# Kernel optimization log

Hardware: AMD Instinct MI355X
Metric: run time of the kernel (lower is better)

## Reference

```python
import jax, jax.numpy as jnp
import numpy as np

D = 256       # video_dim == gcn_dims == interaction_dim
FD = 512      # forward_dim = 2 * interaction_dim
UPDATE_RATE = 0.5


def setup_inputs() -> dict:
    key = jax.random.key(0)
    ks = jax.random.split(key, 20)
    T, N = 768, 384
    s = lambda *sh: 1.0 / np.sqrt(sh[-1])
    return {
        "video_features": jax.random.normal(ks[0], (T, D), jnp.float32),
        "text_features": jax.random.normal(ks[1], (N, D), jnp.float32),
        "video_position_embedding": jax.random.normal(ks[2], (T, D), jnp.float32),
        "text_position_embedding": jax.random.normal(ks[3], (N, D), jnp.float32),
        # VideoEncoder conv1d (out=D, in=D, k=3)
        "conv_w": jax.random.normal(ks[4], (D, D, 3), jnp.float32) * (1.0 / np.sqrt(D * 3)),
        "conv_b": jax.random.normal(ks[5], (D,), jnp.float32) * 0.01,
        # TextGnnEncoder
        "bil_w": jax.random.normal(ks[6], (D, D), jnp.float32) * s(D, D),
        "lin_w": jax.random.normal(ks[7], (D, D), jnp.float32) * s(D, D),
        "lin_b": jax.random.normal(ks[8], (D,), jnp.float32) * 0.01,
        # PairInteraction
        "W1": jax.random.normal(ks[9], (FD, D), jnp.float32) * s(FD, D),
        "b1": jax.random.normal(ks[10], (FD,), jnp.float32) * 0.01,
        "W2": jax.random.normal(ks[11], (FD, D), jnp.float32) * s(FD, D),
        "Wi": jax.random.normal(ks[12], (D, FD), jnp.float32) * s(D, FD),
        "bi": jax.random.normal(ks[13], (D,), jnp.float32) * 0.01,
        # amplifier generators (Linear(interaction_dim, 1))
        "wt": jax.random.normal(ks[14], (D,), jnp.float32) * s(D,),
        "bt": jax.random.normal(ks[15], (1,), jnp.float32) * 0.01,
        "wv": jax.random.normal(ks[16], (D,), jnp.float32) * s(D,),
        "bv": jax.random.normal(ks[17], (1,), jnp.float32) * 0.01,
    }


def _forward(video_features, text_features, video_position_embedding, text_position_embedding,
             conv_w, conv_b, bil_w, lin_w, lin_b, W1, b1, W2, Wi, bi, wt, bt, wv, bv):
    T, N = video_features.shape[0], text_features.shape[0]
    input_video, input_text = video_features, text_features

    v = video_features + video_position_embedding          # (T, D)
    t = text_features + text_position_embedding            # (N, D)

    # VideoEncoder: Conv1d(k=3, pad=1) over time, then ReLU (dropout=0 in eval)
    x = v.T[None]                                           # (1, D, T)
    x = jax.lax.conv_general_dilated(x, conv_w, (1,), [(1, 1)],
                                     dimension_numbers=("NCH", "OIH", "NCH"))
    v = jax.nn.relu(x[0] + conv_b[:, None]).T               # (T, D)

    # TextGnnEncoder
    tn = t / jnp.maximum(jnp.linalg.norm(t, axis=1, keepdims=True), 1e-12)  # L2 normalize rows
    edges = (tn @ bil_w.T) @ tn.T                            # (N, N)
    weights = jax.nn.sigmoid(jnp.mean(edges, axis=1, keepdims=True))        # (N, 1)
    t = weights * (tn @ lin_w.T + lin_b)                     # (N, D)

    # PairInteraction: broadcast add + ReLU + Linear
    f1 = v @ W1.T + b1                                       # (T, FD)
    f2 = t @ W2.T                                            # (N, FD)
    h = jax.nn.relu(f1[:, None, :] + f2[None, :, :])         # (T, N, FD)
    imap = jnp.einsum("tnf,of->tno", h, Wi) + bi             # (T, N, D)

    # dual softmax attention pooling
    text_att = jax.nn.softmax(imap @ wt + bt, axis=1)        # (T, N), softmax over N
    text_context = jnp.einsum("tn,nd->td", text_att, t)      # (T, D)
    video_att = jax.nn.softmax(imap @ wv + bv, axis=0)       # (T, N), softmax over T
    video_context = jnp.einsum("tn,td->nd", video_att, v)    # (N, D)

    ur = UPDATE_RATE
    t_out = video_context * ur + t * (1.0 - ur) + input_text
    v_out = text_context * ur + v * (1.0 - ur) + input_video
    return v_out, t_out


def reference(video_features, text_features, video_position_embedding, text_position_embedding,
              conv_w, conv_b, bil_w, lin_w, lin_b, W1, b1, W2, Wi, bi, wt, bt, wv, bv):
    return _forward(video_features, text_features, video_position_embedding, text_position_embedding,
                    conv_w, conv_b, bil_w, lin_w, lin_b, W1, b1, W2, Wi, bi, wt, bt, wv, bv)
```

## Files before the change

kernel.cpp:

```cpp
#include <hip/hip_runtime.h>
#include <math.h>

#define D  256
#define T  768
#define N  384
#define FD 512

#define DOT4(A,B) ((A).x*(B).x + (A).y*(B).y + (A).z*(B).z + (A).w*(B).w)

__global__ __launch_bounds__(256) void k_front(
    const float* __restrict__ vf, const float* __restrict__ vpos,
    const float* __restrict__ cw, const float* __restrict__ cb,
    const float* __restrict__ tf, const float* __restrict__ tpos,
    const float* __restrict__ Wi, const float* __restrict__ wt,
    const float* __restrict__ wv,
    float* __restrict__ ve, float* __restrict__ tn,
    float* __restrict__ ut, float* __restrict__ uv)
{
    __shared__ float As[34][68];
    __shared__ float Bs[3][32][68];
    const int b = blockIdx.x, tid = threadIdx.x;

    if (b < 192) {
        const int t0 = (b >> 3) * 32;
        const int o0 = (b & 7) * 32;
        const int p  = tid >> 4;
        const int oA = tid & 15;
        float acc00 = 0.f, acc01 = 0.f, acc10 = 0.f, acc11 = 0.f;

        for (int c = 0; c < 4; ++c) {
            const int i0 = c << 6;
            __syncthreads();
#pragma unroll
            for (int s = 0; s < 3; ++s) {
                int u = tid + (s << 8);
                if (u < 544) {
                    int r = u >> 4, uq = u & 15;
                    int gr = t0 - 1 + r;
                    float4 v = make_float4(0.f, 0.f, 0.f, 0.f);
                    if (gr >= 0 && gr < T) {
                        float4 a = *(const float4*)&vf[gr*D + i0 + uq*4];
                        float4 pz = *(const float4*)&vpos[gr*D + i0 + uq*4];
                        v = make_float4(a.x+pz.x, a.y+pz.y, a.z+pz.z, a.w+pz.w);
                    }
                    *(float4*)&As[r][uq*4] = v;
                }
            }
#pragma unroll
            for (int s = 0; s < 6; ++s) {
                int u = tid + (s << 8);
                int oc = u / 48, uq = u - oc * 48;
                float4 v = *(const float4*)&cw[(o0 + oc)*768 + i0*3 + uq*4];
                int j0 = uq * 4;
                Bs[(j0    ) % 3][oc][(j0    ) / 3] = v.x;
                Bs[(j0 + 1) % 3][oc][(j0 + 1) / 3] = v.y;
                Bs[(j0 + 2) % 3][oc][(j0 + 2) / 3] = v.z;
                Bs[(j0 + 3) % 3][oc][(j0 + 3) / 3] = v.w;
            }
            __syncthreads();
#pragma unroll 4
            for (int i4 = 0; i4 < 16; ++i4) {
                float4 ar0 = *(const float4*)&As[2*p    ][i4*4];
                float4 ar1 = *(const float4*)&As[2*p + 1][i4*4];
                float4 ar2 = *(const float4*)&As[2*p + 2][i4*4];
                float4 ar3 = *(const float4*)&As[2*p + 3][i4*4];
                float4 b00 = *(const float4*)&Bs[0][oA   ][i4*4];
                float4 b01 = *(const float4*)&Bs[0][oA+16][i4*4];
                float4 b10 = *(const float4*)&Bs[1][oA   ][i4*4];
                float4 b11 = *(const float4*)&Bs[1][oA+16][i4*4];
                float4 b20 = *(const float4*)&Bs[2][oA   ][i4*4];
                float4 b21 = *(const float4*)&Bs[2][oA+16][i4*4];
                acc00 += DOT4(ar0,b00) + DOT4(ar1,b10) + DOT4(ar2,b20);
                acc01 += DOT4(ar0,b01) + DOT4(ar1,b11) + DOT4(ar2,b21);
                acc10 += DOT4(ar1,b00) + DOT4(ar2,b10) + DOT4(ar3,b20);
                acc11 += DOT4(ar1,b01) + DOT4(ar2,b11) + DOT4(ar3,b21);
            }
        }
        const float bia = cb[o0 + oA], bib = cb[o0 + oA + 16];
        const int t = t0 + 2*p;
        ve[t*D + o0 + oA]          = fmaxf(acc00 + bia, 0.f);
        ve[t*D + o0 + oA + 16]     = fmaxf(acc01 + bib, 0.f);
        ve[(t+1)*D + o0 + oA]      = fmaxf(acc10 + bia, 0.f);
        ve[(t+1)*D + o0 + oA + 16] = fmaxf(acc11 + bib, 0.f);
    } else if (b < 288) {
        const int wid = tid >> 6, lane = tid & 63;
        const int r = (b - 192)*4 + wid;
        float v[4]; float ss = 0.f;
#pragma unroll
        for (int kk = 0; kk < 4; ++kk) {
            v[kk] = tf[r*D + lane + 64*kk] + tpos[r*D + lane + 64*kk];
            ss += v[kk]*v[kk];
        }
#pragma unroll
        for (int off = 1; off < 64; off <<= 1) ss += __shfl_xor(ss, off);
        float inv = 1.0f / fmaxf(sqrtf(ss), 1e-12f);
#pragma unroll
        for (int kk = 0; kk < 4; ++kk) tn[r*D + lane + 64*kk] = v[kk] * inv;
    } else {
        float* wsm = &As[0][0];
        const int which = b - 288;
        const float* w = (which < 2) ? wt : wv;
        float* u = (which < 2) ? ut : uv;
        const int f = ((which & 1) << 8) + tid;
        wsm[tid] = w[tid];
        __syncthreads();
        float s = 0.f;
#pragma unroll 4
        for (int d = 0; d < D; ++d) s += wsm[d] * Wi[d*FD + f];
        u[f] = s;
    }
}

__global__ __launch_bounds__(256) void k_mid(
    const float* __restrict__ ve, const float* __restrict__ W1,
    const float* __restrict__ b1, const float* __restrict__ tn,
    const float* __restrict__ bil, const float* __restrict__ lin_w,
    const float* __restrict__ lin_b,
    float* __restrict__ f1, float* __restrict__ q, float* __restrict__ tl)
{
    __shared__ float As[32][68];
    __shared__ float Bs[32][68];
    const int b = blockIdx.x, tid = threadIdx.x;

    if (b < 384) {
        const int t0 = (b >> 4) * 32;
        const int f0 = (b & 15) * 32;
        const int tA = tid >> 4, fA = tid & 15;
        float acc00 = 0.f, acc01 = 0.f, acc10 = 0.f, acc11 = 0.f;
        for (int c = 0; c < 4; ++c) {
            const int d0 = c << 6;
            __syncthreads();
            const int kc = tid & 63, g = tid >> 6;
#pragma unroll
            for (int it = 0; it < 8; ++it) {
                int tt = g + it*4;
                As[tt][kc] = ve[(t0 + tt)*D + d0 + kc];
                Bs[tt][kc] = W1[(f0 + tt)*D + d0 + kc];
            }
            __syncthreads();
#pragma unroll
            for (int kc4 = 0; kc4 < 16; ++kc4) {
                float4 a0 = *(const float4*)&As[tA][kc4*4];
                float4 a1 = *(const float4*)&As[tA+16][kc4*4];
                float4 b0 = *(const float4*)&Bs[fA][kc4*4];
                float4 b1 = *(const float4*)&Bs[fA+16][kc4*4];
                acc00 += DOT4(a0, b0); acc01 += DOT4(a0, b1);
                acc10 += DOT4(a1, b0); acc11 += DOT4(a1, b1);
            }
        }
        const float bia = b1[f0 + fA], bib = b1[f0 + fA + 16];
        f1[(t0 + tA)*FD + f0 + fA]           = acc00 + bia;
        f1[(t0 + tA)*FD + f0 + fA + 16]      = acc01 + bib;
        f1[(t0 + tA + 16)*FD + f0 + fA]      = acc10 + bia;
        f1[(t0 + tA + 16)*FD + f0 + fA + 16] = acc11 + bib;
    } else if (b < 392) {
        float* tb = &As[0][0];
        float (*qp)[32] = (float(*)[32])&Bs[0][0];
        const int bq = b - 384;
        float s = 0.f;
#pragma unroll 8
        for (int n = 0; n < N; ++n) s += tn[n*D + tid];
        tb[tid] = s * (1.0f / (float)N);
        __syncthreads();
        const int o = tid & 31, dg = tid >> 5;
        float p = 0.f;
#pragma unroll 8
        for (int d = dg*32; d < dg*32 + 32; ++d) p += tb[d] * bil[d*D + bq*32 + o];
        qp[dg][o] = p;
        __syncthreads();
        if (tid < 32) {
            float acc = 0.f;
#pragma unroll
            for (int kk = 0; kk < 8; ++kk) acc += qp[kk][tid];
            q[bq*32 + tid] = acc;
        }
    } else {
        const int bb = b - 392;
        const int n0 = (bb >> 3) * 32;
        const int o0 = (bb & 7) * 32;
        const int tA = tid >> 4, oA = tid & 15;
        float acc00 = 0.f, acc01 = 0.f, acc10 = 0.f, acc11 = 0.f;
        for (int c = 0; c < 4; ++c) {
            const int d0 = c << 6;
            __syncthreads();
            const int kc = tid & 63, g = tid >> 6;
#pragma unroll
            for (int it = 0; it < 8; ++it) {
                int tt = g + it*4;
                As[tt][kc] = tn[(n0 + tt)*D + d0 + kc];
                Bs[tt][kc] = lin_w[(o0 + tt)*D + d0 + kc];
            }
            __syncthreads();
#pragma unroll
            for (int kc4 = 0; kc4 < 16; ++kc4) {
                float4 a0 = *(const float4*)&As[tA][kc4*4];
                float4 a1 = *(const float4*)&As[tA+16][kc4*4];
                float4 b0 = *(const float4*)&Bs[oA][kc4*4];
                float4 b1 = *(const float4*)&Bs[oA+16][kc4*4];
                acc00 += DOT4(a0, b0); acc01 += DOT4(a0, b1);
                acc10 += DOT4(a1, b0); acc11 += DOT4(a1, b1);
            }
        }
        const float bia = lin_b[o0 + oA], bib = lin_b[o0 + oA + 16];
        tl[(n0 + tA)*D + o0 + oA]           = acc00 + bia;
        tl[(n0 + tA)*D + o0 + oA + 16]      = acc01 + bib;
        tl[(n0 + tA + 16)*D + o0 + oA]      = acc10 + bia;
        tl[(n0 + tA + 16)*D + o0 + oA + 16] = acc11 + bib;
    }
}

__global__ __launch_bounds__(256) void k_f2(
    const float* __restrict__ tn, const float* __restrict__ q,
    const float* __restrict__ tl, const float* __restrict__ W2,
    float* __restrict__ tg, float* __restrict__ f2)
{
    __shared__ float As[32][68];
    __shared__ float Bs[32][68];
    __shared__ float wsm[32];
    __shared__ float qs[D];
    const int tid = threadIdx.x;
    const int n0 = (blockIdx.x >> 4) * 32;
    const int f0 = (blockIdx.x & 15) * 32;

    qs[tid] = q[tid];
    __syncthreads();
    {
        const int r = tid >> 3, j = tid & 7;
        const float* row = tn + (n0 + r)*D + j*32;
        float p = 0.f;
#pragma unroll
        for (int m4 = 0; m4 < 8; ++m4) {
            float4 a = *(const float4*)&row[m4*4];
            float4 qq = *(const float4*)&qs[j*32 + m4*4];
            p += DOT4(a, qq);
        }
        p += __shfl_xor(p, 1); p += __shfl_xor(p, 2); p += __shfl_xor(p, 4);
        if (j == 0) wsm[r] = 1.0f / (1.0f + expf(-p));
    }
    __syncthreads();

    const int tA = tid >> 4, fA = tid & 15;
    float acc00 = 0.f, acc01 = 0.f, acc10 = 0.f, acc11 = 0.f;
    for (int c = 0; c < 4; ++c) {
        const int d0 = c << 6;
        __syncthreads();
        const int kc = tid & 63, g = tid >> 6;
#pragma unroll
        for (int it = 0; it < 8; ++it) {
            int tt = g + it*4;
            float av = wsm[tt] * tl[(n0 + tt)*D + d0 + kc];
            As[tt][kc] = av;
            if (f0 == 0) tg[(n0 + tt)*D + d0 + kc] = av;
            Bs[tt][kc] = W2[(f0 + tt)*D + d0 + kc];
        }
        __syncthreads();
#pragma unroll
        for (int kc4 = 0; kc4 < 16; ++kc4) {
            float4 a0 = *(const float4*)&As[tA][kc4*4];
            float4 a1 = *(const float4*)&As[tA+16][kc4*4];
            float4 b0 = *(const float4*)&Bs[fA][kc4*4];
            float4 b1 = *(const float4*)&Bs[fA+16][kc4*4];
            acc00 += DOT4(a0, b0); acc01 += DOT4(a0, b1);
            acc10 += DOT4(a1, b0); acc11 += DOT4(a1, b1);
        }
    }
    f2[(n0 + tA)*FD + f0 + fA]           = acc00;
    f2[(n0 + tA)*FD + f0 + fA + 16]      = acc01;
    f2[(n0 + tA + 16)*FD + f0 + fA]      = acc10;
    f2[(n0 + tA + 16)*FD + f0 + fA + 16] = acc11;
}

__global__ __launch_bounds__(256) void k_score(
    const float* __restrict__ f1, const float* __restrict__ f2,
    const float* __restrict__ ut, const float* __restrict__ uv,
    float* __restrict__ stp, float* __restrict__ svp)
{
    __shared__ float f1s[64][132];
    __shared__ float f2s[32][132];
    __shared__ float us_t[128];
    __shared__ float us_v[128];
    const int tid = threadIdx.x;
    const int t0 = blockIdx.x * 64, n0 = blockIdx.y * 32, c = blockIdx.z;

    if (tid < 128) { us_t[tid] = ut[c*128 + tid]; us_v[tid] = uv[c*128 + tid]; }
#pragma unroll
    for (int s = 0; s < 8; ++s) {
        int j = tid + (s << 8);
        int r = j >> 5, c4 = (j & 31) * 4;
        *(float4*)&f1s[r][c4] = *(const float4*)&f1[(t0 + r)*FD + c*128 + c4];
    }
#pragma unroll
    for (int s = 0; s < 4; ++s) {
        int j = tid + (s << 8);
        int r = j >> 5, c4 = (j & 31) * 4;
        *(float4*)&f2s[r][c4] = *(const float4*)&f2[(n0 + r)*FD + c*128 + c4];
    }
    __syncthreads();

    const int ti = tid >> 4, ni = tid & 15;
    float at[4][2] = {{0.f,0.f},{0.f,0.f},{0.f,0.f},{0.f,0.f}};
    float av[4][2] = {{0.f,0.f},{0.f,0.f},{0.f,0.f},{0.f,0.f}};

#pragma unroll 4
    for (int fq = 0; fq < 32; ++fq) {
        float utv[4], uvv[4], a[4][4], bb[2][4];
        *(float4*)utv   = *(const float4*)&us_t[fq*4];
        *(float4*)uvv   = *(const float4*)&us_v[fq*4];
        *(float4*)a[0]  = *(const float4*)&f1s[ti     ][fq*4];
        *(float4*)a[1]  = *(const float4*)&f1s[ti + 16][fq*4];
        *(float4*)a[2]  = *(const float4*)&f1s[ti + 32][fq*4];
        *(float4*)a[3]  = *(const float4*)&f1s[ti + 48][fq*4];
        *(float4*)bb[0] = *(const float4*)&f2s[ni     ][fq*4];
        *(float4*)bb[1] = *(const float4*)&f2s[ni + 16][fq*4];
#pragma unroll
        for (int e = 0; e < 4; ++e) {
#pragma unroll
            for (int m = 0; m < 4; ++m) {
#pragma unroll
                for (int mn = 0; mn < 2; ++mn) {
                    float h = fmaxf(a[m][e] + bb[mn][e], 0.f);
                    at[m][mn] += h * utv[e];
                    av[m][mn] += h * uvv[e];
                }
            }
        }
    }
    float* stz = stp + c * (T*N);
    float* svz = svp + c * (N*T);
#pragma unroll
    for (int m = 0; m < 4; ++m) {
        const int t = t0 + ti + 16*m;
#pragma unroll
        for (int mn = 0; mn < 2; ++mn) {
            const int n = n0 + ni + 16*mn;
            stz[t*N + n] = at[m][mn];
            svz[n*T + t] = av[m][mn];
        }
    }
}

__global__ __launch_bounds__(256) void k_att(
    const float* __restrict__ stp, const float* __restrict__ svp,
    const float* __restrict__ tg, const float* __restrict__ ve,
    const float* __restrict__ vf, const float* __restrict__ tf,
    float* __restrict__ out_v, float* __restrict__ out_t)
{
    __shared__ float attb[768][4];
    __shared__ float red[4][4];
    __shared__ float ptA[4][4][64];
    __shared__ float ptB[4][4][64];
    const int tid = threadIdx.x;
    const int oo = tid & 63, g = tid >> 6;

    if (blockIdx.x < 384) {
        const int bx = blockIdx.x >> 1, h = blockIdx.x & 1;
        const int t0 = bx * 4;
        const int oA = h*128 + oo, oB = oA + 64;

        float v1[4], v2[4];
#pragma unroll
        for (int r = 0; r < 4; ++r) {
            const float* p = stp + (t0 + r)*N + tid;
            v1[r] = p[0] + p[T*N] + p[2*T*N] + p[3*T*N];
            if (tid < 128) {
                const float* p2 = p + 256;
                v2[r] = p2[0] + p2[T*N] + p2[2*T*N] + p2[3*T*N];
            } else v2[r] = -1e30f;
        }
        float m[4], si[4];
#pragma unroll
        for (int r = 0; r < 4; ++r) {
            float mm = fmaxf(v1[r], v2[r]);
#pragma unroll
            for (int off = 1; off < 64; off <<= 1) mm = fmaxf(mm, __shfl_xor(mm, off));
            if (oo == 0) red[g][r] = mm;
        }
        __syncthreads();
#pragma unroll
        for (int r = 0; r < 4; ++r)
            m[r] = fmaxf(fmaxf(red[0][r], red[1][r]), fmaxf(red[2][r], red[3][r]));
        __syncthreads();
        float e1[4], e2[4];
#pragma unroll
        for (int r = 0; r < 4; ++r) {
            e1[r] = expf(v1[r] - m[r]);
            e2[r] = (tid < 128) ? expf(v2[r] - m[r]) : 0.f;
            float ss = e1[r] + e2[r];
#pragma unroll
            for (int off = 1; off < 64; off <<= 1) ss += __shfl_xor(ss, off);
            if (oo == 0) red[g][r] = ss;
        }
        __syncthreads();
#pragma unroll
        for (int r = 0; r < 4; ++r)
            si[r] = 1.0f / (red[0][r] + red[1][r] + red[2][r] + red[3][r]);
#pragma unroll
        for (int r = 0; r < 4; ++r) {
            attb[tid][r] = e1[r] * si[r];
            if (tid < 128) attb[tid + 256][r] = e2[r] * si[r];
        }
        __syncthreads();

        float accA[4] = {0.f,0.f,0.f,0.f};
        float accB[4] = {0.f,0.f,0.f,0.f};
#pragma unroll 4
        for (int n = g; n < N; n += 4) {
            float4 a0 = *(const float4*)&attb[n][0];
            float tvA = tg[n*D + oA], tvB = tg[n*D + oB];
            accA[0] += a0.x*tvA; accA[1] += a0.y*tvA; accA[2] += a0.z*tvA; accA[3] += a0.w*tvA;
            accB[0] += a0.x*tvB; accB[1] += a0.y*tvB; accB[2] += a0.z*tvB; accB[3] += a0.w*tvB;
        }
#pragma unroll
        for (int r = 0; r < 4; ++r) { ptA[g][r][oo] = accA[r]; ptB[g][r][oo] = accB[r]; }
        __syncthreads();
        if (g < 4) {
            const int rr = g;
            float sA = ptA[0][rr][oo] + ptA[1][rr][oo] + ptA[2][rr][oo] + ptA[3][rr][oo];
            float sB = ptB[0][rr][oo] + ptB[1][rr][oo] + ptB[2][rr][oo] + ptB[3][rr][oo];
            int t = t0 + rr;
            out_v[t*D + oA] = 0.5f*sA + 0.5f*ve[t*D + oA] + vf[t*D + oA];
            out_v[t*D + oB] = 0.5f*sB + 0.5f*ve[t*D + oB] + vf[t*D + oB];
        }
    } else {
        const int b2 = blockIdx.x - 384;
        const int bx = b2 >> 1, h = b2 & 1;
        const int n0 = bx * 4;
        const int oA = h*128 + oo, oB = oA + 64;

        float v1[4], v2[4], v3[4];
#pragma unroll
        for (int r = 0; r < 4; ++r) {
            const float* p = svp + (n0 + r)*T + tid;
            v1[r] = p[0]   + p[N*T]       + p[2*N*T]       + p[3*N*T];
            v2[r] = p[256] + p[N*T + 256] + p[2*N*T + 256] + p[3*N*T + 256];
            v3[r] = p[512] + p[N*T + 512] + p[2*N*T + 512] + p[3*N*T + 512];
        }
        float m[4], si[4];
#pragma unroll
        for (int r = 0; r < 4; ++r) {
            float mm = fmaxf(fmaxf(v1[r], v2[r]), v3[r]);
#pragma unroll
            for (int off = 1; off < 64; off <<= 1) mm = fmaxf(mm, __shfl_xor(mm, off));
            if (oo == 0) red[g][r] = mm;
        }
        __syncthreads();
#pragma unroll
        for (int r = 0; r < 4; ++r)
            m[r] = fmaxf(fmaxf(red[0][r], red[1][r]), fmaxf(red[2][r], red[3][r]));
        __syncthreads();
        float e1[4], e2[4], e3[4];
#pragma unroll
        for (int r = 0; r < 4; ++r) {
            e1[r] = expf(v1[r] - m[r]);
            e2[r] = expf(v2[r] - m[r]);
            e3[r] = expf(v3[r] - m[r]);
            float ss = e1[r] + e2[r] + e3[r];
#pragma unroll
            for (int off = 1; off < 64; off <<= 1) ss += __shfl_xor(ss, off);
            if (oo == 0) red[g][r] = ss;
        }
        __syncthreads();
#pragma unroll
        for (int r = 0; r < 4; ++r)
            si[r] = 1.0f / (red[0][r] + red[1][r] + red[2][r] + red[3][r]);
#pragma unroll
        for (int r = 0; r < 4; ++r) {
            attb[tid][r]       = e1[r] * si[r];
            attb[tid + 256][r] = e2[r] * si[r];
            attb[tid + 512][r] = e3[r] * si[r];
        }
        __syncthreads();

        float accA[4] = {0.f,0.f,0.f,0.f};
        float accB[4] = {0.f,0.f,0.f,0.f};
#pragma unroll 4
        for (int t = g; t < T; t += 4) {
            float4 a0 = *(const float4*)&attb[t][0];
            float vvA = ve[t*D + oA], vvB = ve[t*D + oB];
            accA[0] += a0.x*vvA; accA[1] += a0.y*vvA; accA[2] += a0.z*vvA; accA[3] += a0.w*vvA;
            accB[0] += a0.x*vvB; accB[1] += a0.y*vvB; accB[2] += a0.z*vvB; accB[3] += a0.w*vvB;
        }
#pragma unroll
        for (int r = 0; r < 4; ++r) { ptA[g][r][oo] = accA[r]; ptB[g][r][oo] = accB[r]; }
        __syncthreads();
        if (g < 4) {
            const int rr = g;
            float sA = ptA[0][rr][oo] + ptA[1][rr][oo] + ptA[2][rr][oo] + ptA[3][rr][oo];
            float sB = ptB[0][rr][oo] + ptB[1][rr][oo] + ptB[2][rr][oo] + ptB[3][rr][oo];
            int n = n0 + rr;
            out_t[n*D + oA] = 0.5f*sA + 0.5f*tg[n*D + oA] + tf[n*D + oA];
            out_t[n*D + oB] = 0.5f*sB + 0.5f*tg[n*D + oB] + tf[n*D + oB];
        }
    }
}

extern "C" void kernel_launch(void* const* d_in, const int* in_sizes, int n_in,
                              void* d_out, int out_size, void* d_ws, size_t ws_size,
                              hipStream_t stream)
{
    (void)in_sizes; (void)n_in; (void)out_size; (void)ws_size;
    const float* vf   = (const float*)d_in[0];
    const float* tf   = (const float*)d_in[1];
    const float* vpos = (const float*)d_in[2];
    const float* tpos = (const float*)d_in[3];
    const float* cw   = (const float*)d_in[4];
    const float* cb   = (const float*)d_in[5];
    const float* bil  = (const float*)d_in[6];
    const float* lw   = (const float*)d_in[7];
    const float* lb   = (const float*)d_in[8];
    const float* W1   = (const float*)d_in[9];
    const float* b1   = (const float*)d_in[10];
    const float* W2   = (const float*)d_in[11];
    const float* Wi   = (const float*)d_in[12];
    const float* wt   = (const float*)d_in[14];
    const float* wv   = (const float*)d_in[16];

    float* ws  = (float*)d_ws;
    float* ve  = ws;
    float* tn  = ve + T*D;
    float* tg  = tn + N*D;
    float* tl  = tg + N*D;
    float* f1  = tl + N*D;
    float* f2  = f1 + T*FD;
    float* q   = f2 + N*FD;
    float* ut  = q + D;
    float* uv  = ut + FD;
    float* stp = uv + FD;
    float* svp = stp + 4*T*N;

    float* out_v = (float*)d_out;
    float* out_t = out_v + T*D;

    hipLaunchKernelGGL(k_front, dim3(292),       dim3(256), 0, stream,
                       vf, vpos, cw, cb, tf, tpos, Wi, wt, wv, ve, tn, ut, uv);
    hipLaunchKernelGGL(k_mid,   dim3(488),       dim3(256), 0, stream,
                       ve, W1, b1, tn, bil, lw, lb, f1, q, tl);
    hipLaunchKernelGGL(k_f2,    dim3(192),       dim3(256), 0, stream, tn, q, tl, W2, tg, f2);
    hipLaunchKernelGGL(k_score, dim3(12, 12, 4), dim3(256), 0, stream, f1, f2, ut, uv, stp, svp);
    hipLaunchKernelGGL(k_att,   dim3(576),       dim3(256), 0, stream, stp, svp, tg, ve, vf, tf, out_v, out_t);
}
```

Measured before the change: 102.4 us.

## Restructure pipeline into four kernels with split-K conv and algebraic gate folding

Splits the conv1d over its three taps into separate partial outputs that are summed (with bias and ReLU) when consumed by the W1 GEMM. The text linear is computed from unnormalised text, with normalisation applied as a row scale. The sigmoid gate is folded into f2 inside the score kernel so k_f2 can be removed and the W2 GEMM merged into k_mid. The score kernel moves to 64x64 tiles with 8 FD-chunk partials, which doubles the partial-sum traffic that the attention kernel must read. The goal is fewer launches and more blocks per stage, at the cost of extra workspace traffic and some redundant gate computation.

After: 99.22 us. -3.1%, faster.

```diff
diff --git a/kernel.cpp b/kernel.cpp
--- a/kernel.cpp
+++ b/kernel.cpp
@@ -10,81 +10,73 @@
 
 __global__ __launch_bounds__(256) void k_front(
     const float* __restrict__ vf, const float* __restrict__ vpos,
-    const float* __restrict__ cw, const float* __restrict__ cb,
+    const float* __restrict__ cw,
     const float* __restrict__ tf, const float* __restrict__ tpos,
+    const float* __restrict__ lin_w, const float* __restrict__ lin_b,
     const float* __restrict__ Wi, const float* __restrict__ wt,
     const float* __restrict__ wv,
-    float* __restrict__ ve, float* __restrict__ tn,
-    float* __restrict__ ut, float* __restrict__ uv)
+    float* __restrict__ vep, float* __restrict__ tn,
+    float* __restrict__ tl, float* __restrict__ ut, float* __restrict__ uv)
 {
-    __shared__ float As[34][68];
-    __shared__ float Bs[3][32][68];
+    __shared__ float smem[10880];
     const int b = blockIdx.x, tid = threadIdx.x;
 
-    if (b < 192) {
-        const int t0 = (b >> 3) * 32;
-        const int o0 = (b & 7) * 32;
-        const int p  = tid >> 4;
-        const int oA = tid & 15;
-        float acc00 = 0.f, acc01 = 0.f, acc10 = 0.f, acc11 = 0.f;
+    if (b < 288) {
+        const int k  = b % 3;
+        const int rem = b / 3;
+        const int t0 = (rem % 12) * 64;
+        const int o0 = (rem / 12) * 32;
+        float (*As)[68] = (float(*)[68])smem;
+        float (*Bs)[68] = (float(*)[68])(smem + 4352);
+        const int p = tid >> 4, oi = tid & 15;
+        float a00=0.f,a01=0.f,a10=0.f,a11=0.f,a20=0.f,a21=0.f,a30=0.f,a31=0.f;
 
         for (int c = 0; c < 4; ++c) {
             const int i0 = c << 6;
             __syncthreads();
 #pragma unroll
-            for (int s = 0; s < 3; ++s) {
+            for (int s = 0; s < 4; ++s) {
                 int u = tid + (s << 8);
-                if (u < 544) {
-                    int r = u >> 4, uq = u & 15;
-                    int gr = t0 - 1 + r;
-                    float4 v = make_float4(0.f, 0.f, 0.f, 0.f);
-                    if (gr >= 0 && gr < T) {
-                        float4 a = *(const float4*)&vf[gr*D + i0 + uq*4];
-                        float4 pz = *(const float4*)&vpos[gr*D + i0 + uq*4];
-                        v = make_float4(a.x+pz.x, a.y+pz.y, a.z+pz.z, a.w+pz.w);
-                    }
-                    *(float4*)&As[r][uq*4] = v;
+                int r = u >> 4, q4 = (u & 15) * 4;
+                int gr = t0 + r + k - 1;
+                float4 v = make_float4(0.f,0.f,0.f,0.f);
+                if (gr >= 0 && gr < T) {
+                    float4 x = *(const float4*)&vf[gr*D + i0 + q4];
+                    float4 y = *(const float4*)&vpos[gr*D + i0 + q4];
+                    v = make_float4(x.x+y.x, x.y+y.y, x.z+y.z, x.w+y.w);
                 }
-            }
-#pragma unroll
-            for (int s = 0; s < 6; ++s) {
+                *(float4*)&As[r][q4] = v;
+            }
+#pragma unroll
+            for (int s = 0; s < 8; ++s) {
                 int u = tid + (s << 8);
-                int oc = u / 48, uq = u - oc * 48;
-                float4 v = *(const float4*)&cw[(o0 + oc)*768 + i0*3 + uq*4];
-                int j0 = uq * 4;
-                Bs[(j0    ) % 3][oc][(j0    ) / 3] = v.x;
-                Bs[(j0 + 1) % 3][oc][(j0 + 1) / 3] = v.y;
-                Bs[(j0 + 2) % 3][oc][(j0 + 2) / 3] = v.z;
-                Bs[(j0 + 3) % 3][oc][(j0 + 3) / 3] = v.w;
+                int o = u >> 6, i = u & 63;
+                Bs[o][i] = cw[(o0 + o)*768 + (i0 + i)*3 + k];
             }
             __syncthreads();
 #pragma unroll 4
-            for (int i4 = 0; i4 < 16; ++i4) {
-                float4 ar0 = *(const float4*)&As[2*p    ][i4*4];
-                float4 ar1 = *(const float4*)&As[2*p + 1][i4*4];
-                float4 ar2 = *(const float4*)&As[2*p + 2][i4*4];
-                float4 ar3 = *(const float4*)&As[2*p + 3][i4*4];
-                float4 b00 = *(const float4*)&Bs[0][oA   ][i4*4];
-                float4 b01 = *(const float4*)&Bs[0][oA+16][i4*4];
-                float4 b10 = *(const float4*)&Bs[1][oA   ][i4*4];
-                float4 b11 = *(const float4*)&Bs[1][oA+16][i4*4];
-                float4 b20 = *(const float4*)&Bs[2][oA   ][i4*4];
-                float4 b21 = *(const float4*)&Bs[2][oA+16][i4*4];
-                acc00 += DOT4(ar0,b00) + DOT4(ar1,b10) + DOT4(ar2,b20);
-                acc01 += DOT4(ar0,b01) + DOT4(ar1,b11) + DOT4(ar2,b21);
-                acc10 += DOT4(ar1,b00) + DOT4(ar2,b10) + DOT4(ar3,b20);
-                acc11 += DOT4(ar1,b01) + DOT4(ar2,b11) + DOT4(ar3,b21);
-            }
-        }
-        const float bia = cb[o0 + oA], bib = cb[o0 + oA + 16];
-        const int t = t0 + 2*p;
-        ve[t*D + o0 + oA]          = fmaxf(acc00 + bia, 0.f);
-        ve[t*D + o0 + oA + 16]     = fmaxf(acc01 + bib, 0.f);
-        ve[(t+1)*D + o0 + oA]      = fmaxf(acc10 + bia, 0.f);
-        ve[(t+1)*D + o0 + oA + 16] = fmaxf(acc11 + bib, 0.f);
-    } else if (b < 288) {
+            for (int kc4 = 0; kc4 < 16; ++kc4) {
+                float4 r0 = *(const float4*)&As[4*p    ][kc4*4];
+                float4 r1 = *(const float4*)&As[4*p + 1][kc4*4];
+                float4 r2 = *(const float4*)&As[4*p + 2][kc4*4];
+                float4 r3 = *(const float4*)&As[4*p + 3][kc4*4];
+                float4 b0 = *(const float4*)&Bs[oi     ][kc4*4];
+                float4 b1 = *(const float4*)&Bs[oi + 16][kc4*4];
+                a00 += DOT4(r0,b0); a01 += DOT4(r0,b1);
+                a10 += DOT4(r1,b0); a11 += DOT4(r1,b1);
+                a20 += DOT4(r2,b0); a21 += DOT4(r2,b1);
+                a30 += DOT4(r3,b0); a31 += DOT4(r3,b1);
+            }
+        }
+        float* vz = vep + k * (T*D);
+        const int t = t0 + 4*p;
+        vz[(t  )*D + o0 + oi] = a00;  vz[(t  )*D + o0 + oi + 16] = a01;
+        vz[(t+1)*D + o0 + oi] = a10;  vz[(t+1)*D + o0 + oi + 16] = a11;
+        vz[(t+2)*D + o0 + oi] = a20;  vz[(t+2)*D + o0 + oi + 16] = a21;
+        vz[(t+3)*D + o0 + oi] = a30;  vz[(t+3)*D + o0 + oi + 16] = a31;
+    } else if (b < 384) {
         const int wid = tid >> 6, lane = tid & 63;
-        const int r = (b - 192)*4 + wid;
+        const int r = (b - 288)*4 + wid;
         float v[4]; float ss = 0.f;
 #pragma unroll
         for (int kk = 0; kk < 4; ++kk) {
@@ -96,9 +88,64 @@
         float inv = 1.0f / fmaxf(sqrtf(ss), 1e-12f);
 #pragma unroll
         for (int kk = 0; kk < 4; ++kk) tn[r*D + lane + 64*kk] = v[kk] * inv;
+    } else if (b < 480) {
+        const int bb = b - 384;
+        const int n0 = (bb >> 3) * 32;
+        const int o0 = (bb & 7) * 32;
+        float (*As2)[260] = (float(*)[260])smem;
+        float (*Bs2)[68]  = (float(*)[68])(smem + 8320);
+        float* inv = smem + 10496;
+#pragma unroll
+        for (int s = 0; s < 8; ++s) {
+            int u = tid + (s << 8);
+            int r = u >> 6, q4 = (u & 63) * 4;
+            float4 x = *(const float4*)&tf[(n0 + r)*D + q4];
+            float4 y = *(const float4*)&tpos[(n0 + r)*D + q4];
+            *(float4*)&As2[r][q4] = make_float4(x.x+y.x, x.y+y.y, x.z+y.z, x.w+y.w);
+        }
+        __syncthreads();
+        {
+            const int r = tid >> 3, j = tid & 7;
+            float p = 0.f;
+#pragma unroll
+            for (int m = 0; m < 8; ++m) {
+                float4 a = *(const float4*)&As2[r][j*32 + m*4];
+                p += DOT4(a, a);
+            }
+            p += __shfl_xor(p, 1); p += __shfl_xor(p, 2); p += __shfl_xor(p, 4);
+            if (j == 0) inv[r] = 1.0f / fmaxf(sqrtf(p), 1e-12f);
+        }
+        const int tA = tid >> 4, oA = tid & 15;
+        float acc00=0.f, acc01=0.f, acc10=0.f, acc11=0.f;
+        for (int c = 0; c < 4; ++c) {
+            const int d0 = c << 6;
+            __syncthreads();
+#pragma unroll
+            for (int s = 0; s < 2; ++s) {
+                int u = tid + (s << 8);
+                int o = u >> 4, q4 = (u & 15) * 4;
+                *(float4*)&Bs2[o][q4] = *(const float4*)&lin_w[(o0 + o)*D + d0 + q4];
+            }
+            __syncthreads();
+#pragma unroll 4
+            for (int kc4 = 0; kc4 < 16; ++kc4) {
+                float4 a0 = *(const float4*)&As2[tA     ][d0 + kc4*4];
+                float4 a1 = *(const float4*)&As2[tA + 16][d0 + kc4*4];
+                float4 b0 = *(const float4*)&Bs2[oA     ][kc4*4];
+                float4 b1 = *(const float4*)&Bs2[oA + 16][kc4*4];
+                acc00 += DOT4(a0,b0); acc01 += DOT4(a0,b1);
+                acc10 += DOT4(a1,b0); acc11 += DOT4(a1,b1);
+            }
+        }
+        const float i0n = inv[tA], i1n = inv[tA + 16];
+        const float lb0 = lin_b[o0 + oA], lb1 = lin_b[o0 + oA + 16];
+        tl[(n0 + tA     )*D + o0 + oA]      = i0n*acc00 + lb0;
+        tl[(n0 + tA     )*D + o0 + oA + 16] = i0n*acc01 + lb1;
+        tl[(n0 + tA + 16)*D + o0 + oA]      = i1n*acc10 + lb0;
+        tl[(n0 + tA + 16)*D + o0 + oA + 16] = i1n*acc11 + lb1;
     } else {
-        float* wsm = &As[0][0];
-        const int which = b - 288;
+        float* wsm = smem;
+        const int which = b - 480;
         const float* w = (which < 2) ? wt : wv;
         float* u = (which < 2) ? ut : uv;
         const int f = ((which & 1) << 8) + tid;
@@ -112,50 +159,102 @@
 }
 
 __global__ __launch_bounds__(256) void k_mid(
-    const float* __restrict__ ve, const float* __restrict__ W1,
-    const float* __restrict__ b1, const float* __restrict__ tn,
-    const float* __restrict__ bil, const float* __restrict__ lin_w,
-    const float* __restrict__ lin_b,
-    float* __restrict__ f1, float* __restrict__ q, float* __restrict__ tl)
+    const float* __restrict__ vep, const float* __restrict__ cbp,
+    const float* __restrict__ W1, const float* __restrict__ b1v,
+    const float* __restrict__ tlp, const float* __restrict__ W2,
+    const float* __restrict__ tn, const float* __restrict__ bil,
+    float* __restrict__ f1, float* __restrict__ f2,
+    float* __restrict__ ve, float* __restrict__ q)
 {
-    __shared__ float As[32][68];
-    __shared__ float Bs[32][68];
+    __shared__ float smem[6656];
     const int b = blockIdx.x, tid = threadIdx.x;
 
-    if (b < 384) {
-        const int t0 = (b >> 4) * 32;
-        const int f0 = (b & 15) * 32;
-        const int tA = tid >> 4, fA = tid & 15;
-        float acc00 = 0.f, acc01 = 0.f, acc10 = 0.f, acc11 = 0.f;
+    if (b < 288) {
+        const bool isF1 = (b < 192);
+        const int bb = isF1 ? b : b - 192;
+        const int nT = isF1 ? 12 : 6;
+        const int r0 = (bb % nT) * 64;
+        const int f0 = (bb / nT) * 32;
+        float (*As)[68] = (float(*)[68])smem;
+        float (*Bs)[68] = (float(*)[68])(smem + 4352);
+        const int p = tid >> 4, fi = tid & 15;
+        float a00=0.f,a01=0.f,a10=0.f,a11=0.f,a20=0.f,a21=0.f,a30=0.f,a31=0.f;
+        const float* Wp = isF1 ? W1 : W2;
+
         for (int c = 0; c < 4; ++c) {
             const int d0 = c << 6;
             __syncthreads();
-            const int kc = tid & 63, g = tid >> 6;
-#pragma unroll
-            for (int it = 0; it < 8; ++it) {
-                int tt = g + it*4;
-                As[tt][kc] = ve[(t0 + tt)*D + d0 + kc];
-                Bs[tt][kc] = W1[(f0 + tt)*D + d0 + kc];
+            if (isF1) {
+#pragma unroll
+                for (int s = 0; s < 4; ++s) {
+                    int u = tid + (s << 8);
+                    int r = u >> 4, q4 = (u & 15) * 4;
+                    const int off = (r0 + r)*D + d0 + q4;
+                    float4 p0 = *(const float4*)&vep[off];
+                    float4 p1 = *(const float4*)&vep[T*D + off];
+                    float4 p2 = *(const float4*)&vep[2*T*D + off];
+                    float4 cbv = *(const float4*)&cbp[d0 + q4];
+                    float4 v;
+                    v.x = fmaxf(p0.x+p1.x+p2.x+cbv.x, 0.f);
+                    v.y = fmaxf(p0.y+p1.y+p2.y+cbv.y, 0.f);
+                    v.z = fmaxf(p0.z+p1.z+p2.z+cbv.z, 0.f);
+                    v.w = fmaxf(p0.w+p1.w+p2.w+cbv.w, 0.f);
+                    *(float4*)&As[r][q4] = v;
+                }
+            } else {
+#pragma unroll
+                for (int s = 0; s < 4; ++s) {
+                    int u = tid + (s << 8);
+                    int r = u >> 4, q4 = (u & 15) * 4;
+                    *(float4*)&As[r][q4] = *(const float4*)&tlp[(r0 + r)*D + d0 + q4];
+                }
+            }
+#pragma unroll
+            for (int s = 0; s < 2; ++s) {
+                int u = tid + (s << 8);
+                int o = u >> 4, q4 = (u & 15) * 4;
+                *(float4*)&Bs[o][q4] = *(const float4*)&Wp[(f0 + o)*D + d0 + q4];
             }
             __syncthreads();
-#pragma unroll
+#pragma unroll 4
             for (int kc4 = 0; kc4 < 16; ++kc4) {
-                float4 a0 = *(const float4*)&As[tA][kc4*4];
-                float4 a1 = *(const float4*)&As[tA+16][kc4*4];
-                float4 b0 = *(const float4*)&Bs[fA][kc4*4];
-                float4 b1 = *(const float4*)&Bs[fA+16][kc4*4];
-                acc00 += DOT4(a0, b0); acc01 += DOT4(a0, b1);
-                acc10 += DOT4(a1, b0); acc11 += DOT4(a1, b1);
-            }
-        }
-        const float bia = b1[f0 + fA], bib = b1[f0 + fA + 16];
-        f1[(t0 + tA)*FD + f0 + fA]           = acc00 + bia;
-        f1[(t0 + tA)*FD + f0 + fA + 16]      = acc01 + bib;
-        f1[(t0 + tA + 16)*FD + f0 + fA]      = acc10 + bia;
-        f1[(t0 + tA + 16)*FD + f0 + fA + 16] = acc11 + bib;
-    } else if (b < 392) {
-        float* tb = &As[0][0];
-        float (*qp)[32] = (float(*)[32])&Bs[0][0];
+                float4 r0v = *(const float4*)&As[4*p    ][kc4*4];
+                float4 r1v = *(const float4*)&As[4*p + 1][kc4*4];
+                float4 r2v = *(const float4*)&As[4*p + 2][kc4*4];
+                float4 r3v = *(const float4*)&As[4*p + 3][kc4*4];
+                float4 b0 = *(const float4*)&Bs[fi     ][kc4*4];
+                float4 b1 = *(const float4*)&Bs[fi + 16][kc4*4];
+                a00 += DOT4(r0v,b0); a01 += DOT4(r0v,b1);
+                a10 += DOT4(r1v,b0); a11 += DOT4(r1v,b1);
+                a20 += DOT4(r2v,b0); a21 += DOT4(r2v,b1);
+                a30 += DOT4(r3v,b0); a31 += DOT4(r3v,b1);
+            }
+        }
+        const int r = r0 + 4*p;
+        if (isF1) {
+            const float bi0 = b1v[f0 + fi], bi1 = b1v[f0 + fi + 16];
+            f1[(r  )*FD + f0 + fi] = a00 + bi0;  f1[(r  )*FD + f0 + fi + 16] = a01 + bi1;
+            f1[(r+1)*FD + f0 + fi] = a10 + bi0;  f1[(r+1)*FD + f0 + fi + 16] = a11 + bi1;
+            f1[(r+2)*FD + f0 + fi] = a20 + bi0;  f1[(r+2)*FD + f0 + fi + 16] = a21 + bi1;
+            f1[(r+3)*FD + f0 + fi] = a30 + bi0;  f1[(r+3)*FD + f0 + fi + 16] = a31 + bi1;
+        } else {
+            f2[(r  )*FD + f0 + fi] = a00;  f2[(r  )*FD + f0 + fi + 16] = a01;
+            f2[(r+1)*FD + f0 + fi] = a10;  f2[(r+1)*FD + f0 + fi + 16] = a11;
+            f2[(r+2)*FD + f0 + fi] = a20;  f2[(r+2)*FD + f0 + fi + 16] = a21;
+            f2[(r+3)*FD + f0 + fi] = a30;  f2[(r+3)*FD + f0 + fi + 16] = a31;
+        }
+    } else if (b < 384) {
+        const int t0 = (b - 288) * 8;
+        float cbv = cbp[tid];
+#pragma unroll
+        for (int r = 0; r < 8; ++r) {
+            const int off = (t0 + r)*D + tid;
+            float s = vep[off] + vep[T*D + off] + vep[2*T*D + off] + cbv;
+            ve[off] = fmaxf(s, 0.f);
+        }
+    } else {
+        float* tb = smem;
+        float (*qp)[32] = (float(*)[32])(smem + 256);
         const int bq = b - 384;
         float s = 0.f;
 #pragma unroll 8
@@ -174,168 +273,129 @@
             for (int kk = 0; kk < 8; ++kk) acc += qp[kk][tid];
             q[bq*32 + tid] = acc;
         }
-    } else {
-        const int bb = b - 392;
-        const int n0 = (bb >> 3) * 32;
-        const int o0 = (bb & 7) * 32;
-        const int tA = tid >> 4, oA = tid & 15;
-        float acc00 = 0.f, acc01 = 0.f, acc10 = 0.f, acc11 = 0.f;
-        for (int c = 0; c < 4; ++c) {
-            const int d0 = c << 6;
-            __syncthreads();
-            const int kc = tid & 63, g = tid >> 6;
-#pragma unroll
-            for (int it = 0; it < 8; ++it) {
-                int tt = g + it*4;
-                As[tt][kc] = tn[(n0 + tt)*D + d0 + kc];
-                Bs[tt][kc] = lin_w[(o0 + tt)*D + d0 + kc];
-            }
-            __syncthreads();
-#pragma unroll
-            for (int kc4 = 0; kc4 < 16; ++kc4) {
-                float4 a0 = *(const float4*)&As[tA][kc4*4];
-                float4 a1 = *(const float4*)&As[tA+16][kc4*4];
-                float4 b0 = *(const float4*)&Bs[oA][kc4*4];
-                float4 b1 = *(const float4*)&Bs[oA+16][kc4*4];
-                acc00 += DOT4(a0, b0); acc01 += DOT4(a0, b1);
-                acc10 += DOT4(a1, b0); acc11 += DOT4(a1, b1);
-            }
-        }
-        const float bia = lin_b[o0 + oA], bib = lin_b[o0 + oA + 16];
-        tl[(n0 + tA)*D + o0 + oA]           = acc00 + bia;
-        tl[(n0 + tA)*D + o0 + oA + 16]      = acc01 + bib;
-        tl[(n0 + tA + 16)*D + o0 + oA]      = acc10 + bia;
-        tl[(n0 + tA + 16)*D + o0 + oA + 16] = acc11 + bib;
     }
 }
 
-__global__ __launch_bounds__(256) void k_f2(
-    const float* __restrict__ tn, const float* __restrict__ q,
-    const float* __restrict__ tl, const float* __restrict__ W2,
-    float* __restrict__ tg, float* __restrict__ f2)
-{
-    __shared__ float As[32][68];
-    __shared__ float Bs[32][68];
-    __shared__ float wsm[32];
-    __shared__ float qs[D];
-    const int tid = threadIdx.x;
-    const int n0 = (blockIdx.x >> 4) * 32;
-    const int f0 = (blockIdx.x & 15) * 32;
-
-    qs[tid] = q[tid];
-    __syncthreads();
-    {
-        const int r = tid >> 3, j = tid & 7;
-        const float* row = tn + (n0 + r)*D + j*32;
-        float p = 0.f;
-#pragma unroll
-        for (int m4 = 0; m4 < 8; ++m4) {
-            float4 a = *(const float4*)&row[m4*4];
-            float4 qq = *(const float4*)&qs[j*32 + m4*4];
-            p += DOT4(a, qq);
-        }
-        p += __shfl_xor(p, 1); p += __shfl_xor(p, 2); p += __shfl_xor(p, 4);
-        if (j == 0) wsm[r] = 1.0f / (1.0f + expf(-p));
-    }
-    __syncthreads();
-
-    const int tA = tid >> 4, fA = tid & 15;
-    float acc00 = 0.f, acc01 = 0.f, acc10 = 0.f, acc11 = 0.f;
-    for (int c = 0; c < 4; ++c) {
-        const int d0 = c << 6;
-        __syncthreads();
-        const int kc = tid & 63, g = tid >> 6;
-#pragma unroll
-        for (int it = 0; it < 8; ++it) {
-            int tt = g + it*4;
-            float av = wsm[tt] * tl[(n0 + tt)*D + d0 + kc];
-            As[tt][kc] = av;
-            if (f0 == 0) tg[(n0 + tt)*D + d0 + kc] = av;
-            Bs[tt][kc] = W2[(f0 + tt)*D + d0 + kc];
-        }
-        __syncthreads();
-#pragma unroll
-        for (int kc4 = 0; kc4 < 16; ++kc4) {
-            float4 a0 = *(const float4*)&As[tA][kc4*4];
-            float4 a1 = *(const float4*)&As[tA+16][kc4*4];
-            float4 b0 = *(const float4*)&Bs[fA][kc4*4];
-            float4 b1 = *(const float4*)&Bs[fA+16][kc4*4];
-            acc00 += DOT4(a0, b0); acc01 += DOT4(a0, b1);
-            acc10 += DOT4(a1, b0); acc11 += DOT4(a1, b1);
-        }
-    }
-    f2[(n0 + tA)*FD + f0 + fA]           = acc00;
-    f2[(n0 + tA)*FD + f0 + fA + 16]      = acc01;
-    f2[(n0 + tA + 16)*FD + f0 + fA]      = acc10;
-    f2[(n0 + tA + 16)*FD + f0 + fA + 16] = acc11;
-}
-
 __global__ __launch_bounds__(256) void k_score(
     const float* __restrict__ f1, const float* __restrict__ f2,
+    const float* __restrict__ tn, const float* __restrict__ qv,
+    const float* __restrict__ tlp,
     const float* __restrict__ ut, const float* __restrict__ uv,
-    float* __restrict__ stp, float* __restrict__ svp)
+    float* __restrict__ stp, float* __restrict__ svp, float* __restrict__ tg)
 {
-    __shared__ float f1s[64][132];
-    __shared__ float f2s[32][132];
-    __shared__ float us_t[128];
-    __shared__ float us_v[128];
+    __shared__ float smem[9216];
     const int tid = threadIdx.x;
-    const int t0 = blockIdx.x * 64, n0 = blockIdx.y * 32, c = blockIdx.z;
-
-    if (tid < 128) { us_t[tid] = ut[c*128 + tid]; us_v[tid] = uv[c*128 + tid]; }
-#pragma unroll
-    for (int s = 0; s < 8; ++s) {
-        int j = tid + (s << 8);
-        int r = j >> 5, c4 = (j & 31) * 4;
-        *(float4*)&f1s[r][c4] = *(const float4*)&f1[(t0 + r)*FD + c*128 + c4];
-    }
-#pragma unroll
-    for (int s = 0; s < 4; ++s) {
-        int j = tid + (s << 8);
-        int r = j >> 5, c4 = (j & 31) * 4;
-        *(float4*)&f2s[r][c4] = *(const float4*)&f2[(n0 + r)*FD + c*128 + c4];
-    }
-    __syncthreads();
-
-    const int ti = tid >> 4, ni = tid & 15;
-    float at[4][2] = {{0.f,0.f},{0.f,0.f},{0.f,0.f},{0.f,0.f}};
-    float av[4][2] = {{0.f,0.f},{0.f,0.f},{0.f,0.f},{0.f,0.f}};
-
-#pragma unroll 4
-    for (int fq = 0; fq < 32; ++fq) {
-        float utv[4], uvv[4], a[4][4], bb[2][4];
-        *(float4*)utv   = *(const float4*)&us_t[fq*4];
-        *(float4*)uvv   = *(const float4*)&us_v[fq*4];
-        *(float4*)a[0]  = *(const float4*)&f1s[ti     ][fq*4];
-        *(float4*)a[1]  = *(const float4*)&f1s[ti + 16][fq*4];
-        *(float4*)a[2]  = *(const float4*)&f1s[ti + 32][fq*4];
-        *(float4*)a[3]  = *(const float4*)&f1s[ti + 48][fq*4];
-        *(float4*)bb[0] = *(const float4*)&f2s[ni     ][fq*4];
-        *(float4*)bb[1] = *(const float4*)&f2s[ni + 16][fq*4];
-#pragma unroll
-        for (int e = 0; e < 4; ++e) {
-#pragma unroll
-            for (int m = 0; m < 4; ++m) {
-#pragma unroll
-                for (int mn = 0; mn < 2; ++mn) {
-                    float h = fmaxf(a[m][e] + bb[mn][e], 0.f);
-                    at[m][mn] += h * utv[e];
-                    av[m][mn] += h * uvv[e];
+    const int bid = blockIdx.x;
+
+    if (bid < 576) {
+        const int t0 = (bid % 12) * 64;
+        const int n0 = ((bid / 12) % 6) * 64;
+        const int iz = bid / 72;
+        const int fz = iz * 64;
+        float (*f1s)[68] = (float(*)[68])smem;
+        float (*f2s)[68] = (float(*)[68])(smem + 4352);
+        float* qs   = smem + 8704;
+        float* us_t = smem + 8960;
+        float* us_v = smem + 9024;
+        float* wsm  = smem + 9088;
+
+        qs[tid] = qv[tid];
+        if (tid < 64) us_t[tid] = ut[fz + tid];
+        else if (tid < 128) us_v[tid - 64] = uv[fz + tid - 64];
+        __syncthreads();
+        {
+            const int r = tid >> 2, j = tid & 3;
+            float p = 0.f;
+#pragma unroll
+            for (int m = 0; m < 16; ++m) {
+                float4 a = *(const float4*)&tn[(n0 + r)*D + j*64 + m*4];
+                float4 qq = *(const float4*)&qs[j*64 + m*4];
+                p += DOT4(a, qq);
+            }
+            p += __shfl_xor(p, 1); p += __shfl_xor(p, 2);
+            if (j == 0) wsm[r] = 1.0f / (1.0f + expf(-p));
+        }
+#pragma unroll
+        for (int s = 0; s < 4; ++s) {
+            int u = tid + (s << 8);
+            int r = u >> 4, q4 = (u & 15) * 4;
+            *(float4*)&f1s[r][q4] = *(const float4*)&f1[(t0 + r)*FD + fz + q4];
+        }
+        __syncthreads();
+#pragma unroll
+        for (int s = 0; s < 4; ++s) {
+            int u = tid + (s << 8);
+            int r = u >> 4, q4 = (u & 15) * 4;
+            float w = wsm[r];
+            float4 v = *(const float4*)&f2[(n0 + r)*FD + fz + q4];
+            *(float4*)&f2s[r][q4] = make_float4(w*v.x, w*v.y, w*v.z, w*v.w);
+        }
+        __syncthreads();
+
+        const int ti = tid >> 4, ni = tid & 15;
+        float at[4][4], av[4][4];
+#pragma unroll
+        for (int i = 0; i < 4; ++i)
+#pragma unroll
+            for (int j = 0; j < 4; ++j) { at[i][j] = 0.f; av[i][j] = 0.f; }
+
+#pragma unroll 2
+        for (int fq = 0; fq < 16; ++fq) {
+            float a[4][4], bb[4][4], utv[4], uvv[4];
+            *(float4*)utv  = *(const float4*)&us_t[fq*4];
+            *(float4*)uvv  = *(const float4*)&us_v[fq*4];
+#pragma unroll
+            for (int i = 0; i < 4; ++i) {
+                *(float4*)a[i]  = *(const float4*)&f1s[ti + 16*i][fq*4];
+                *(float4*)bb[i] = *(const float4*)&f2s[ni + 16*i][fq*4];
+            }
+#pragma unroll
+            for (int e = 0; e < 4; ++e) {
+#pragma unroll
+                for (int i = 0; i < 4; ++i) {
+#pragma unroll
+                    for (int j = 0; j < 4; ++j) {
+                        float h = fmaxf(a[i][e] + bb[j][e], 0.f);
+                        at[i][j] += h * utv[e];
+                        av[i][j] += h * uvv[e];
+                    }
                 }
             }
         }
-    }
-    float* stz = stp + c * (T*N);
-    float* svz = svp + c * (N*T);
-#pragma unroll
-    for (int m = 0; m < 4; ++m) {
-        const int t = t0 + ti + 16*m;
-#pragma unroll
-        for (int mn = 0; mn < 2; ++mn) {
-            const int n = n0 + ni + 16*mn;
-            stz[t*N + n] = at[m][mn];
-            svz[n*T + t] = av[m][mn];
-        }
+        float* stz = stp + iz * (T*N);
+        float* svz = svp + iz * (N*T);
+#pragma unroll
+        for (int i = 0; i < 4; ++i) {
+            const int t = t0 + ti + 16*i;
+#pragma unroll
+            for (int j = 0; j < 4; ++j) {
+                const int n = n0 + ni + 16*j;
+                stz[t*N + n] = at[i][j];
+                svz[n*T + t] = av[i][j];
+            }
+        }
+    } else {
+        const int n0 = (bid - 576) * 32;
+        float* qs  = smem;
+        float* wsm = smem + 256;
+        qs[tid] = qv[tid];
+        __syncthreads();
+        {
+            const int r = tid >> 3, j = tid & 7;
+            float p = 0.f;
+#pragma unroll
+            for (int m = 0; m < 8; ++m) {
+                float4 a = *(const float4*)&tn[(n0 + r)*D + j*32 + m*4];
+                float4 qq = *(const float4*)&qs[j*32 + m*4];
+                p += DOT4(a, qq);
+            }
+            p += __shfl_xor(p, 1); p += __shfl_xor(p, 2); p += __shfl_xor(p, 4);
+            if (j == 0) wsm[r] = 1.0f / (1.0f + expf(-p));
+        }
+        __syncthreads();
+#pragma unroll
+        for (int r = 0; r < 32; ++r)
+            tg[(n0 + r)*D + tid] = wsm[r] * tlp[(n0 + r)*D + tid];
     }
 }
 
@@ -351,6 +411,7 @@
     __shared__ float ptB[4][4][64];
     const int tid = threadIdx.x;
     const int oo = tid & 63, g = tid >> 6;
+    const int TN = T*N;
 
     if (blockIdx.x < 384) {
         const int bx = blockIdx.x >> 1, h = blockIdx.x & 1;
@@ -361,10 +422,15 @@
 #pragma unroll
         for (int r = 0; r < 4; ++r) {
             const float* p = stp + (t0 + r)*N + tid;
-            v1[r] = p[0] + p[T*N] + p[2*T*N] + p[3*T*N];
+            float s1 = 0.f;
+#pragma unroll
+            for (int z = 0; z < 8; ++z) s1 += p[z*TN];
+            v1[r] = s1;
             if (tid < 128) {
-                const float* p2 = p + 256;
-                v2[r] = p2[0] + p2[T*N] + p2[2*T*N] + p2[3*T*N];
+                float s2 = 0.f;
+#pragma unroll
+                for (int z = 0; z < 8; ++z) s2 += p[z*TN + 256];
+                v2[r] = s2;
             } else v2[r] = -1e30f;
         }
         float m[4], si[4];
@@ -431,9 +497,14 @@
 #pragma unroll
         for (int r = 0; r < 4; ++r) {
             const float* p = svp + (n0 + r)*T + tid;
-            v1[r] = p[0]   + p[N*T]       + p[2*N*T]       + p[3*N*T];
-            v2[r] = p[256] + p[N*T + 256] + p[2*N*T + 256] + p[3*N*T + 256];
-            v3[r] = p[512] + p[N*T + 512] + p[2*N*T + 512] + p[3*N*T + 512];
+            float s1 = 0.f, s2 = 0.f, s3 = 0.f;
+#pragma unroll
+            for (int z = 0; z < 8; ++z) {
+                s1 += p[z*TN];
+                s2 += p[z*TN + 256];
+                s3 += p[z*TN + 512];
+            }
+            v1[r] = s1; v2[r] = s2; v3[r] = s3;
         }
         float m[4], si[4];
 #pragma unroll
@@ -516,26 +587,28 @@
     const float* wv   = (const float*)d_in[16];
 
     float* ws  = (float*)d_ws;
-    float* ve  = ws;
+    float* vep = ws;
+    float* ve  = vep + 3*T*D;
     float* tn  = ve + T*D;
-    float* tg  = tn + N*D;
-    float* tl  = tg + N*D;
-    float* f1  = tl + N*D;
+    float* tl  = tn + N*D;
+    float* tg  = tl + N*D;
+    float* f1  = tg + N*D;
     float* f2  = f1 + T*FD;
     float* q   = f2 + N*FD;
     float* ut  = q + D;
     float* uv  = ut + FD;
     float* stp = uv + FD;
-    float* svp = stp + 4*T*N;
+    float* svp = stp + 8*T*N;
 
     float* out_v = (float*)d_out;
     float* out_t = out_v + T*D;
 
-    hipLaunchKernelGGL(k_front, dim3(292),       dim3(256), 0, stream,
-                       vf, vpos, cw, cb, tf, tpos, Wi, wt, wv, ve, tn, ut, uv);
-    hipLaunchKernelGGL(k_mid,   dim3(488),       dim3(256), 0, stream,
-                       ve, W1, b1, tn, bil, lw, lb, f1, q, tl);
-    hipLaunchKernelGGL(k_f2,    dim3(192),       dim3(256), 0, stream, tn, q, tl, W2, tg, f2);
-    hipLaunchKernelGGL(k_score, dim3(12, 12, 4), dim3(256), 0, stream, f1, f2, ut, uv, stp, svp);
-    hipLaunchKernelGGL(k_att,   dim3(576),       dim3(256), 0, stream, stp, svp, tg, ve, vf, tf, out_v, out_t);
+    hipLaunchKernelGGL(k_front, dim3(484), dim3(256), 0, stream,
+                       vf, vpos, cw, tf, tpos, lw, lb, Wi, wt, wv, vep, tn, tl, ut, uv);
+    hipLaunchKernelGGL(k_mid,   dim3(392), dim3(256), 0, stream,
+                       vep, cb, W1, b1, tl, W2, tn, bil, f1, f2, ve, q);
+    hipLaunchKernelGGL(k_score, dim3(588), dim3(256), 0, stream,
+                       f1, f2, tn, q, tl, ut, uv, stp, svp, tg);
+    hipLaunchKernelGGL(k_att,   dim3(576), dim3(256), 0, stream,
+                       stp, svp, tg, ve, vf, tf, out_v, out_t);
 }
```
